# Kernel optimization log

Measured on AMD Instinct MI355X. Metric: run time of the kernel, lower is better.

The kernel has to match this reference:

```python
import jax, jax.numpy as jnp
import numpy as np

PS = 8  # patch_size
EPS = 1e-5


def _layernorm(t, w, b):
    m = jnp.mean(t, axis=-1, keepdims=True)
    v = jnp.mean((t - m) ** 2, axis=-1, keepdims=True)
    return (t - m) * jax.lax.rsqrt(v + EPS) * w + b


def _to3d(t):  # B(HW)C -> BCHW
    B, N, C = t.shape
    H = W = int(np.sqrt(N))
    return t.reshape(B, H, W, C).transpose(0, 3, 1, 2)


def _to2d(t):  # BCHW -> B(HW)C
    B, C, H, W = t.shape
    return t.reshape(B, C, H * W).swapaxes(-1, -2)


def _block(t, ps=PS):  # BCHW -> [B, M, ps*ps, C] (dilated-grid blocking, as in torch code)
    B, C, H, W = t.shape
    t = t.reshape(B, C, ps, H // ps, ps, W // ps)
    t = t.transpose(0, 3, 5, 2, 4, 1)
    return t.reshape(B, (H * W) // (ps * ps), ps * ps, C)


def _unblock(t):  # inverse of _block
    B, M, N, C = t.shape
    Hb = Wb = int(np.sqrt(M))
    ps = int(np.sqrt(N))
    t = t.reshape(B, Hb, Wb, ps, ps, C)
    t = t.transpose(0, 5, 3, 1, 4, 2)
    return t.reshape(B, C, Hb * ps, Wb * ps)


def setup_inputs() -> dict:
    key = jax.random.key(0)
    ks = jax.random.split(key, 8)
    B, N, D, H = 8, 4096, 256, 8
    s = 1.0 / np.sqrt(D)
    return {
        "x": jax.random.normal(ks[0], (B, N, D), jnp.float32),
        "ln1_w": jnp.ones((D,), jnp.float32),
        "ln1_b": jnp.zeros((D,), jnp.float32),
        "q": jax.random.normal(ks[1], (H, D, D), jnp.float32) * s,
        "k": jax.random.normal(ks[2], (D, D), jnp.float32) * s,
        "v": jax.random.normal(ks[3], (D, D), jnp.float32) * s,
        "o": jax.random.normal(ks[4], (H, D, D), jnp.float32) * s,
        "ln2_w": jnp.ones((D,), jnp.float32),
        "ln2_b": jnp.zeros((D,), jnp.float32),
        "w1": jax.random.normal(ks[5], (D, D), jnp.float32) * s,
        "b1": jnp.zeros((D,), jnp.float32),
        "w2": jax.random.normal(ks[6], (D, D), jnp.float32) * s,
        "b2": jnp.zeros((D,), jnp.float32),
    }


def reference(x, ln1_w, ln1_b, q, k, v, o, ln2_w, ln2_b, w1, b1, w2, b2):
    # blocked input: [B, M, P, D], M = HW/ps^2, P = ps^2
    a = _block(_to3d(_layernorm(x, ln1_w, ln1_b)))
    nh = q.shape[0]
    Q = jnp.einsum('bmnd,hdk->bhmnk', a, q)
    Q1, Q2 = Q[:, : nh // 2], Q[:, nh // 2 :]
    K = jnp.einsum('bmnd,dk->bmnk', a, k)
    V = jnp.einsum('bmnd,dv->bmnv', a, v)
    # axis 1: attend across blocks (m) at fixed within-block position (y=n)
    s1 = jax.nn.softmax(jnp.einsum('bhxyk,bzyk->bhyxz', Q1, K), axis=-1)
    O1 = jnp.einsum('bhyxz,bzyv->bhxyv', s1, V)
    # axis 2: attend within block (n) at fixed block (x=m)
    s2 = jax.nn.softmax(jnp.einsum('bhxyk,bxzk->bhxyz', Q2, K), axis=-1)
    O2 = jnp.einsum('bhxyz,bxzv->bhxyv', s2, V)
    O = jnp.concatenate([O1, O2], axis=1)  # [B, H, M, P, D]
    # faithful to torch: 'bhmnd,hdv->bmnd' sums over h and v
    Z = jnp.einsum('bhmnd,hdv->bmnd', O, o)
    x = x + _to2d(_unblock(Z))
    h = _layernorm(x, ln2_w, ln2_b)
    mlp = jax.nn.relu(h @ w1 + b1) @ w2 + b2
    return x + mlp
```

## Files before the change

### kernel.cpp

```cpp
#include <hip/hip_runtime.h>

#define Bc   8
#define Tc   4096
#define Dc   256
#define EPSc 1e-5f

typedef _Float16 half_t;
typedef __attribute__((ext_vector_type(4))) _Float16 half4_t;
typedef __attribute__((ext_vector_type(8))) _Float16 frag8;
typedef __attribute__((ext_vector_type(4))) float f32x4;

#define MFMA_F16(a, b, c) __builtin_amdgcn_mfma_f32_16x16x32_f16((a), (b), (c), 0, 0, 0)

__global__ __launch_bounds__(256) void osum_kernel(const float* __restrict__ o, float* __restrict__ os) {
  int h = blockIdx.x, d = threadIdx.x;
  const float* row = o + ((size_t)h * 256 + d) * 256;
  float s = 0.f;
  #pragma unroll 8
  for (int v = 0; v < 256; v += 4) {
    float4 r4 = *(const float4*)&row[v];
    s += r4.x + r4.y + r4.z + r4.w;
  }
  os[h * 256 + d] = s;
}

__global__ __launch_bounds__(256) void prepM_kernel(const float* __restrict__ q,
                                                    const float* __restrict__ k,
                                                    half_t* __restrict__ Mt) {
  __shared__ float shK[32 * 260];
  __shared__ float shQ[32 * 260];
  int tid = threadIdx.x;
  int h = blockIdx.x >> 6, et = (blockIdx.x >> 3) & 7, dt = blockIdx.x & 7;
  const float* kbase = k + (size_t)(et * 32) * 256;
  const float* qbase = q + ((size_t)h * 256 + dt * 32) * 256;
  #pragma unroll
  for (int r = 0; r < 8; r++) {
    int f = r * 256 + tid;
    int row = f >> 6, c4 = (f & 63) * 4;
    *(float4*)&shK[row * 260 + c4] = *(const float4*)&kbase[(size_t)row * 256 + c4];
    *(float4*)&shQ[row * 260 + c4] = *(const float4*)&qbase[(size_t)row * 256 + c4];
  }
  __syncthreads();
  int e = tid & 31, dg = tid >> 5;
  const float* kr = &shK[e * 260];
  const float* q0 = &shQ[(dg * 4 + 0) * 260];
  const float* q1 = &shQ[(dg * 4 + 1) * 260];
  const float* q2 = &shQ[(dg * 4 + 2) * 260];
  const float* q3 = &shQ[(dg * 4 + 3) * 260];
  float a0 = 0.f, a1 = 0.f, a2 = 0.f, a3 = 0.f;
  #pragma unroll 4
  for (int kk = 0; kk < 256; kk += 4) {
    float4 kv = *(const float4*)&kr[kk];
    float4 v0 = *(const float4*)&q0[kk];
    float4 v1 = *(const float4*)&q1[kk];
    float4 v2 = *(const float4*)&q2[kk];
    float4 v3 = *(const float4*)&q3[kk];
    a0 += v0.x * kv.x + v0.y * kv.y + v0.z * kv.z + v0.w * kv.w;
    a1 += v1.x * kv.x + v1.y * kv.y + v1.z * kv.z + v1.w * kv.w;
    a2 += v2.x * kv.x + v2.y * kv.y + v2.z * kv.z + v2.w * kv.w;
    a3 += v3.x * kv.x + v3.y * kv.y + v3.z * kv.z + v3.w * kv.w;
  }
  half4_t outv;
  outv[0] = (half_t)a0; outv[1] = (half_t)a1; outv[2] = (half_t)a2; outv[3] = (half_t)a3;
  *(half4_t*)&Mt[((size_t)h * 256 + et * 32 + e) * 256 + dt * 32 + dg * 4] = outv;
}

__global__ __launch_bounds__(256) void prepT_kernel(const float* __restrict__ v,
                                                    const float* __restrict__ w1,
                                                    const float* __restrict__ w2,
                                                    half_t* vt, half_t* w1t, half_t* w2t) {
  int which = blockIdx.x >> 8, n = blockIdx.x & 255, d = threadIdx.x;
  const float* src = which == 0 ? v : (which == 1 ? w1 : w2);
  half_t* dst = which == 0 ? vt : (which == 1 ? w1t : w2t);
  dst[(size_t)n * 256 + d] = (half_t)src[(size_t)d * 256 + n];
}

__global__ __launch_bounds__(256) void ln1_kernel(
    const float* __restrict__ x, const float* __restrict__ w,
    const float* __restrict__ bia, half_t* __restrict__ aH) {
  int row  = blockIdx.x * 4 + (threadIdx.x >> 6);
  int lane = threadIdx.x & 63;
  float4 v = *(const float4*)&x[(size_t)row * 256 + lane * 4];
  float s  = v.x + v.y + v.z + v.w;
  float sq = v.x * v.x + v.y * v.y + v.z * v.z + v.w * v.w;
  #pragma unroll
  for (int off = 1; off < 64; off <<= 1) { s += __shfl_xor(s, off); sq += __shfl_xor(sq, off); }
  float mean = s * (1.f / 256), var = sq * (1.f / 256) - mean * mean;
  float r = rsqrtf(var + EPSc);
  float4 wv = *(const float4*)&w[lane * 4];
  float4 bv = *(const float4*)&bia[lane * 4];
  half4_t y;
  y[0] = (half_t)((v.x - mean) * r * wv.x + bv.x);
  y[1] = (half_t)((v.y - mean) * r * wv.y + bv.y);
  y[2] = (half_t)((v.z - mean) * r * wv.z + bv.z);
  y[3] = (half_t)((v.w - mean) * r * wv.w + bv.w);
  int bb = row >> 12, p = row & 4095, hh = p >> 6, ww = p & 63;
  int m = (hh & 7) * 8 + (ww & 7), n = (hh >> 3) * 8 + (ww >> 3);
  *(half4_t*)&aH[((size_t)((bb * 64 + m) * 64 + n)) * 256 + lane * 4] = y;
}

__global__ __launch_bounds__(256, 2) void attn_kernel(
    const half_t* __restrict__ aH, const half_t* __restrict__ Mt,
    const half_t* __restrict__ vt, const float* __restrict__ osum,
    half_t* __restrict__ Z0, half_t* __restrict__ Z1, int gofs) {
  __shared__ half_t shA[64 * 264];
  __shared__ half_t shU[64 * 264 + 64 * 72];
  half_t* shVT = shU;
  half_t* shW  = shU;
  half_t* shP  = shU + 64 * 264;
  int tid = threadIdx.x, lane = tid & 63, w = tid >> 6;
  int l16 = lane & 15, quad = lane >> 4;
  int g = blockIdx.x + gofs;
  int mode = g >> 9, gg = g & 511, b = gg >> 6, slice = gg & 63;
  int hbase = mode * 4;
  half_t* Z = mode ? Z1 : Z0;

  #pragma unroll
  for (int i = 0; i < 8; i++) {
    int slot = i * 256 + tid;
    int z = slot >> 5, c8 = (slot & 31) * 8;
    size_t rz = mode ? ((size_t)(b * 64 + slice) * 64 + z) : ((size_t)(b * 64 + z) * 64 + slice);
    *(frag8*)&shA[z * 264 + c8] = *(const frag8*)&aH[rz * 256 + c8];
  }
  __syncthreads();

  #pragma unroll
  for (int dth = 0; dth < 2; dth++) {
    f32x4 vacc[2][4];
    #pragma unroll
    for (int dt2 = 0; dt2 < 2; dt2++)
      #pragma unroll
      for (int zt = 0; zt < 4; zt++) vacc[dt2][zt] = (f32x4){0.f, 0.f, 0.f, 0.f};
    #pragma unroll
    for (int ks = 0; ks < 8; ks++) {
      int k0 = ks * 32 + quad * 8;
      frag8 vf0 = *(const frag8*)&vt[(size_t)(w * 64 + dth * 32 +  0 + l16) * 256 + k0];
      frag8 vf1 = *(const frag8*)&vt[(size_t)(w * 64 + dth * 32 + 16 + l16) * 256 + k0];
      frag8 bfr[4];
      #pragma unroll
      for (int zt = 0; zt < 4; zt++)
        bfr[zt] = *(const frag8*)&shA[(zt * 16 + l16) * 264 + k0];
      #pragma unroll
      for (int zt = 0; zt < 4; zt++) {
        vacc[0][zt] = MFMA_F16(vf0, bfr[zt], vacc[0][zt]);
        vacc[1][zt] = MFMA_F16(vf1, bfr[zt], vacc[1][zt]);
      }
    }
    #pragma unroll
    for (int dt2 = 0; dt2 < 2; dt2++)
      #pragma unroll
      for (int zt = 0; zt < 4; zt++)
        #pragma unroll
        for (int r = 0; r < 4; r++)
          shVT[(w * 64 + dth * 32 + dt2 * 16 + quad * 4 + r) * 72 + zt * 16 + l16] = (half_t)vacc[dt2][zt][r];
  }
  __syncthreads();

  frag8 vtreg[4][2];
  #pragma unroll
  for (int dt = 0; dt < 4; dt++)
    #pragma unroll
    for (int ks = 0; ks < 2; ks++)
      vtreg[dt][ks] = *(const frag8*)&shVT[(w * 64 + dt * 16 + l16) * 72 + ks * 32 + quad * 8];

  float osv[4][4];
  #pragma unroll
  for (int hh = 0; hh < 4; hh++)
    #pragma unroll
    for (int dt = 0; dt < 4; dt++)
      osv[hh][dt] = osum[(hbase + hh) * 256 + w * 64 + dt * 16 + l16];

  f32x4 zacc[4][4];
  #pragma unroll
  for (int mf = 0; mf < 4; mf++)
    #pragma unroll
    for (int dt = 0; dt < 4; dt++) zacc[mf][dt] = (f32x4){0.f, 0.f, 0.f, 0.f};
  __syncthreads();

  #pragma unroll
  for (int hh = 0; hh < 4; hh++) {
    const half_t* Mth = Mt + (size_t)(hbase + hh) * 65536;
    #pragma unroll
    for (int eh = 0; eh < 2; eh++) {
      f32x4 wacc[2][4];
      #pragma unroll
      for (int et2 = 0; et2 < 2; et2++)
        #pragma unroll
        for (int mf = 0; mf < 4; mf++) wacc[et2][mf] = (f32x4){0.f, 0.f, 0.f, 0.f};
      #pragma unroll
      for (int ks = 0; ks < 8; ks++) {
        int k0 = ks * 32 + quad * 8;
        frag8 bf0 = *(const frag8*)&Mth[(size_t)(w * 64 + eh * 32 +  0 + l16) * 256 + k0];
        frag8 bf1 = *(const frag8*)&Mth[(size_t)(w * 64 + eh * 32 + 16 + l16) * 256 + k0];
        frag8 af[4];
        #pragma unroll
        for (int mf = 0; mf < 4; mf++) af[mf] = *(const frag8*)&shA[(mf * 16 + l16) * 264 + k0];
        #pragma unroll
        for (int mf = 0; mf < 4; mf++) {
          wacc[0][mf] = MFMA_F16(af[mf], bf0, wacc[0][mf]);
          wacc[1][mf] = MFMA_F16(af[mf], bf1, wacc[1][mf]);
        }
      }
      #pragma unroll
      for (int et2 = 0; et2 < 2; et2++)
        #pragma unroll
        for (int mf = 0; mf < 4; mf++)
          #pragma unroll
          for (int r = 0; r < 4; r++)
            shW[(mf * 16 + quad * 4 + r) * 264 + w * 64 + eh * 32 + et2 * 16 + l16] = (half_t)wacc[et2][mf][r];
    }
    __syncthreads();
    {
      f32x4 sacc[4];
      #pragma unroll
      for (int zt = 0; zt < 4; zt++) sacc[zt] = (f32x4){0.f, 0.f, 0.f, 0.f};
      #pragma unroll
      for (int ks = 0; ks < 8; ks++) {
        int k0 = ks * 32 + quad * 8;
        frag8 wf = *(const frag8*)&shW[(w * 16 + l16) * 264 + k0];
        #pragma unroll
        for (int zt = 0; zt < 4; zt++) {
          frag8 kf = *(const frag8*)&shA[(zt * 16 + l16) * 264 + k0];
          sacc[zt] = MFMA_F16(wf, kf, sacc[zt]);
        }
      }
      #pragma unroll
      for (int r = 0; r < 4; r++) {
        float mx = fmaxf(fmaxf(sacc[0][r], sacc[1][r]), fmaxf(sacc[2][r], sacc[3][r]));
        #pragma unroll
        for (int off = 1; off < 16; off <<= 1) mx = fmaxf(mx, __shfl_xor(mx, off));
        float e0 = __expf(sacc[0][r] - mx), e1 = __expf(sacc[1][r] - mx);
        float e2 = __expf(sacc[2][r] - mx), e3 = __expf(sacc[3][r] - mx);
        float sum = e0 + e1 + e2 + e3;
        #pragma unroll
        for (int off = 1; off < 16; off <<= 1) sum += __shfl_xor(sum, off);
        float inv = 1.f / sum;
        int m = w * 16 + quad * 4 + r;
        shP[m * 72 + l16 +  0] = (half_t)(e0 * inv);
        shP[m * 72 + l16 + 16] = (half_t)(e1 * inv);
        shP[m * 72 + l16 + 32] = (half_t)(e2 * inv);
        shP[m * 72 + l16 + 48] = (half_t)(e3 * inv);
      }
    }
    __syncthreads();
    #pragma unroll
    for (int mf = 0; mf < 4; mf++) {
      frag8 pf0 = *(const frag8*)&shP[(mf * 16 + l16) * 72 +  0 + quad * 8];
      frag8 pf1 = *(const frag8*)&shP[(mf * 16 + l16) * 72 + 32 + quad * 8];
      #pragma unroll
      for (int dt = 0; dt < 4; dt++) {
        f32x4 oacc = (f32x4){0.f, 0.f, 0.f, 0.f};
        oacc = MFMA_F16(pf0, vtreg[dt][0], oacc);
        oacc = MFMA_F16(pf1, vtreg[dt][1], oacc);
        #pragma unroll
        for (int r = 0; r < 4; r++) zacc[mf][dt][r] += oacc[r] * osv[hh][dt];
      }
    }
  }

  #pragma unroll
  for (int mf = 0; mf < 4; mf++)
    #pragma unroll
    for (int dt = 0; dt < 4; dt++)
      #pragma unroll
      for (int r = 0; r < 4; r++)
        shA[(mf * 16 + quad * 4 + r) * 264 + w * 64 + dt * 16 + l16] = (half_t)zacc[mf][dt][r];
  __syncthreads();
  #pragma unroll
  for (int i = 0; i < 8; i++) {
    int slot = i * 256 + tid;
    int grow = slot >> 5, c8 = (slot & 31) * 8;
    size_t zrow = mode ? ((size_t)(b * 64 + slice) * 64 + grow) : ((size_t)(b * 64 + grow) * 64 + slice);
    *(frag8*)&Z[zrow * 256 + c8] = *(const frag8*)&shA[grow * 264 + c8];
  }
}

__global__ __launch_bounds__(256, 2) void mlp_kernel(
    const float* __restrict__ x, const half_t* __restrict__ Z0, const half_t* __restrict__ Z1,
    const float* __restrict__ lw, const float* __restrict__ lb,
    const half_t* __restrict__ w1t, const float* __restrict__ b1,
    const half_t* __restrict__ w2t, const float* __restrict__ b2,
    float* __restrict__ out) {
  __shared__ half_t shH[64 * 264];
  __shared__ half_t shHH[64 * 264];
  int tid = threadIdx.x, lane = tid & 63, w = tid >> 6;
  int l16 = lane & 15, quad = lane >> 4;
  int row0 = blockIdx.x * 64;

  #pragma unroll 4
  for (int i = 0; i < 16; i++) {
    int rl = w * 16 + i;
    int row = row0 + rl;
    size_t base = (size_t)row * 256 + lane * 4;
    int bb = row >> 12, p = row & 4095, hh = p >> 6, ww = p & 63;
    int m = (hh & 7) * 8 + (ww & 7), n = (hh >> 3) * 8 + (ww >> 3);
    size_t zbase = ((size_t)((bb * 64 + m) * 64 + n)) * 256 + lane * 4;
    float4 xv = *(const float4*)&x[base];
    half4_t zv0 = *(const half4_t*)&Z0[zbase];
    half4_t zv1 = *(const half4_t*)&Z1[zbase];
    float4 v;
    v.x = xv.x + (float)zv0[0] + (float)zv1[0];
    v.y = xv.y + (float)zv0[1] + (float)zv1[1];
    v.z = xv.z + (float)zv0[2] + (float)zv1[2];
    v.w = xv.w + (float)zv0[3] + (float)zv1[3];
    float s  = v.x + v.y + v.z + v.w;
    float sq = v.x * v.x + v.y * v.y + v.z * v.z + v.w * v.w;
    #pragma unroll
    for (int off = 1; off < 64; off <<= 1) { s += __shfl_xor(s, off); sq += __shfl_xor(sq, off); }
    float mean = s * (1.f / 256), var = sq * (1.f / 256) - mean * mean;
    float r = rsqrtf(var + EPSc);
    float4 wv = *(const float4*)&lw[lane * 4];
    float4 bv = *(const float4*)&lb[lane * 4];
    half4_t y;
    y[0] = (half_t)((v.x - mean) * r * wv.x + bv.x);
    y[1] = (half_t)((v.y - mean) * r * wv.y + bv.y);
    y[2] = (half_t)((v.z - mean) * r * wv.z + bv.z);
    y[3] = (half_t)((v.w - mean) * r * wv.w + bv.w);
    *(half4_t*)&shH[rl * 264 + lane * 4] = y;
  }
  __syncthreads();

  {
    f32x4 acc[4][4];
    #pragma unroll
    for (int mf = 0; mf < 4; mf++)
      #pragma unroll
      for (int nt = 0; nt < 4; nt++) acc[mf][nt] = (f32x4){0.f, 0.f, 0.f, 0.f};
    #pragma unroll
    for (int ks = 0; ks < 8; ks++) {
      int k0 = ks * 32 + quad * 8;
      frag8 af[4], bf[4];
      #pragma unroll
      for (int mf = 0; mf < 4; mf++) af[mf] = *(const frag8*)&shH[(mf * 16 + l16) * 264 + k0];
      #pragma unroll
      for (int nt = 0; nt < 4; nt++)
        bf[nt] = *(const frag8*)&w1t[(size_t)(w * 64 + nt * 16 + l16) * 256 + k0];
      #pragma unroll
      for (int mf = 0; mf < 4; mf++)
        #pragma unroll
        for (int nt = 0; nt < 4; nt++) acc[mf][nt] = MFMA_F16(af[mf], bf[nt], acc[mf][nt]);
    }
    #pragma unroll
    for (int mf = 0; mf < 4; mf++)
      #pragma unroll
      for (int nt = 0; nt < 4; nt++)
        #pragma unroll
        for (int r = 0; r < 4; r++) {
          int rr = mf * 16 + quad * 4 + r, col = w * 64 + nt * 16 + l16;
          float vv = acc[mf][nt][r] + b1[col];
          vv = fmaxf(vv, 0.f);
          shHH[rr * 264 + col] = (half_t)vv;
        }
  }
  __syncthreads();

  {
    f32x4 acc[4][4];
    #pragma unroll
    for (int mf = 0; mf < 4; mf++)
      #pragma unroll
      for (int nt = 0; nt < 4; nt++) acc[mf][nt] = (f32x4){0.f, 0.f, 0.f, 0.f};
    #pragma unroll
    for (int ks = 0; ks < 8; ks++) {
      int k0 = ks * 32 + quad * 8;
      frag8 af[4], bf[4];
      #pragma unroll
      for (int mf = 0; mf < 4; mf++) af[mf] = *(const frag8*)&shHH[(mf * 16 + l16) * 264 + k0];
      #pragma unroll
      for (int nt = 0; nt < 4; nt++)
        bf[nt] = *(const frag8*)&w2t[(size_t)(w * 64 + nt * 16 + l16) * 256 + k0];
      #pragma unroll
      for (int mf = 0; mf < 4; mf++)
        #pragma unroll
        for (int nt = 0; nt < 4; nt++) acc[mf][nt] = MFMA_F16(af[mf], bf[nt], acc[mf][nt]);
    }
    #pragma unroll
    for (int mf = 0; mf < 4; mf++)
      #pragma unroll
      for (int r = 0; r < 4; r++) {
        int rr = mf * 16 + quad * 4 + r;
        int row = row0 + rr;
        int bb = row >> 12, p = row & 4095, hh = p >> 6, ww = p & 63;
        int m = (hh & 7) * 8 + (ww & 7), n = (hh >> 3) * 8 + (ww >> 3);
        size_t zrow = ((size_t)((bb * 64 + m) * 64 + n)) * 256;
        size_t xrow = (size_t)row * 256;
        #pragma unroll
        for (int nt = 0; nt < 4; nt++) {
          int col = w * 64 + nt * 16 + l16;
          float vres = x[xrow + col] + (float)Z0[zrow + col] + (float)Z1[zrow + col];
          float vv = acc[mf][nt][r] + b2[col];
          out[xrow + col] = vv + vres;
        }
      }
  }
}

extern "C" void kernel_launch(void* const* d_in, const int* in_sizes, int n_in,
                              void* d_out, int out_size, void* d_ws, size_t ws_size,
                              hipStream_t stream) {
  (void)in_sizes; (void)n_in; (void)out_size; (void)ws_size;
  const float* x    = (const float*)d_in[0];
  const float* ln1w = (const float*)d_in[1];
  const float* ln1b = (const float*)d_in[2];
  const float* q    = (const float*)d_in[3];
  const float* k    = (const float*)d_in[4];
  const float* v    = (const float*)d_in[5];
  const float* o    = (const float*)d_in[6];
  const float* ln2w = (const float*)d_in[7];
  const float* ln2b = (const float*)d_in[8];
  const float* w1   = (const float*)d_in[9];
  const float* b1   = (const float*)d_in[10];
  const float* w2   = (const float*)d_in[11];
  const float* b2   = (const float*)d_in[12];
  float* out = (float*)d_out;

  const size_t ROWS = (size_t)Bc * Tc;
  const size_t ELTS = ROWS * Dc;
  const size_t MB16 = ELTS * sizeof(half_t);
  char* ws = (char*)d_ws;
  float*  osumB = (float*)ws;
  half_t* Mt    = (half_t*)(ws + (64 << 10));
  half_t* vt    = (half_t*)(ws + (64 << 10) + (1 << 20));
  half_t* w1t   = (half_t*)(ws + (64 << 10) + (1 << 20) + (128 << 10));
  half_t* w2t   = (half_t*)(ws + (64 << 10) + (1 << 20) + (256 << 10));
  half_t* aH    = (half_t*)(ws + (2 << 20));
  half_t* Zb0   = (half_t*)(ws + (2 << 20) + MB16);
  half_t* Zb1   = (half_t*)(ws + (2 << 20) + 2 * MB16);

  osum_kernel <<<8,   256, 0, stream>>>(o, osumB);
  prepM_kernel<<<512, 256, 0, stream>>>(q, k, Mt);
  prepT_kernel<<<768, 256, 0, stream>>>(v, w1, w2, vt, w1t, w2t);
  ln1_kernel  <<<ROWS / 4, 256, 0, stream>>>(x, ln1w, ln1b, aH);
  attn_kernel <<<1024, 256, 0, stream>>>(aH, Mt, vt, osumB, Zb0, Zb1, 0);
  mlp_kernel  <<<ROWS / 64, 256, 0, stream>>>(x, Zb0, Zb1, ln2w, ln2b, w1t, b1, w2t, b2, out);
}
```

Measured before the change: 276.9 us.

## Fuse LayerNorm1 into attention load and merge weight-prep kernels into one launch

```diff
diff --git a/kernel.cpp b/kernel.cpp
--- a/kernel.cpp
+++ b/kernel.cpp
@@ -12,97 +12,71 @@
 
 #define MFMA_F16(a, b, c) __builtin_amdgcn_mfma_f32_16x16x32_f16((a), (b), (c), 0, 0, 0)
 
-__global__ __launch_bounds__(256) void osum_kernel(const float* __restrict__ o, float* __restrict__ os) {
-  int h = blockIdx.x, d = threadIdx.x;
-  const float* row = o + ((size_t)h * 256 + d) * 256;
-  float s = 0.f;
-  #pragma unroll 8
-  for (int v = 0; v < 256; v += 4) {
-    float4 r4 = *(const float4*)&row[v];
-    s += r4.x + r4.y + r4.z + r4.w;
-  }
-  os[h * 256 + d] = s;
-}
-
-__global__ __launch_bounds__(256) void prepM_kernel(const float* __restrict__ q,
-                                                    const float* __restrict__ k,
-                                                    half_t* __restrict__ Mt) {
+__global__ __launch_bounds__(256) void prep_kernel(
+    const float* __restrict__ q, const float* __restrict__ k,
+    const float* __restrict__ v, const float* __restrict__ w1, const float* __restrict__ w2,
+    const float* __restrict__ o,
+    half_t* __restrict__ Mt, half_t* vt, half_t* w1t, half_t* w2t, float* __restrict__ os) {
   __shared__ float shK[32 * 260];
   __shared__ float shQ[32 * 260];
-  int tid = threadIdx.x;
-  int h = blockIdx.x >> 6, et = (blockIdx.x >> 3) & 7, dt = blockIdx.x & 7;
-  const float* kbase = k + (size_t)(et * 32) * 256;
-  const float* qbase = q + ((size_t)h * 256 + dt * 32) * 256;
-  #pragma unroll
-  for (int r = 0; r < 8; r++) {
-    int f = r * 256 + tid;
-    int row = f >> 6, c4 = (f & 63) * 4;
-    *(float4*)&shK[row * 260 + c4] = *(const float4*)&kbase[(size_t)row * 256 + c4];
-    *(float4*)&shQ[row * 260 + c4] = *(const float4*)&qbase[(size_t)row * 256 + c4];
-  }
-  __syncthreads();
-  int e = tid & 31, dg = tid >> 5;
-  const float* kr = &shK[e * 260];
-  const float* q0 = &shQ[(dg * 4 + 0) * 260];
-  const float* q1 = &shQ[(dg * 4 + 1) * 260];
-  const float* q2 = &shQ[(dg * 4 + 2) * 260];
-  const float* q3 = &shQ[(dg * 4 + 3) * 260];
-  float a0 = 0.f, a1 = 0.f, a2 = 0.f, a3 = 0.f;
-  #pragma unroll 4
-  for (int kk = 0; kk < 256; kk += 4) {
-    float4 kv = *(const float4*)&kr[kk];
-    float4 v0 = *(const float4*)&q0[kk];
-    float4 v1 = *(const float4*)&q1[kk];
-    float4 v2 = *(const float4*)&q2[kk];
-    float4 v3 = *(const float4*)&q3[kk];
-    a0 += v0.x * kv.x + v0.y * kv.y + v0.z * kv.z + v0.w * kv.w;
-    a1 += v1.x * kv.x + v1.y * kv.y + v1.z * kv.z + v1.w * kv.w;
-    a2 += v2.x * kv.x + v2.y * kv.y + v2.z * kv.z + v2.w * kv.w;
-    a3 += v3.x * kv.x + v3.y * kv.y + v3.z * kv.z + v3.w * kv.w;
-  }
-  half4_t outv;
-  outv[0] = (half_t)a0; outv[1] = (half_t)a1; outv[2] = (half_t)a2; outv[3] = (half_t)a3;
-  *(half4_t*)&Mt[((size_t)h * 256 + et * 32 + e) * 256 + dt * 32 + dg * 4] = outv;
+  int bid = blockIdx.x, tid = threadIdx.x;
+  if (bid < 512) {
+    int h = bid >> 6, et = (bid >> 3) & 7, dt = bid & 7;
+    const float* kbase = k + (size_t)(et * 32) * 256;
+    const float* qbase = q + ((size_t)h * 256 + dt * 32) * 256;
+    #pragma unroll
+    for (int r = 0; r < 8; r++) {
+      int f = r * 256 + tid;
+      int row = f >> 6, c4 = (f & 63) * 4;
+      *(float4*)&shK[row * 260 + c4] = *(const float4*)&kbase[(size_t)row * 256 + c4];
+      *(float4*)&shQ[row * 260 + c4] = *(const float4*)&qbase[(size_t)row * 256 + c4];
+    }
+    __syncthreads();
+    int e = tid & 31, dg = tid >> 5;
+    const float* kr = &shK[e * 260];
+    const float* q0 = &shQ[(dg * 4 + 0) * 260];
+    const float* q1 = &shQ[(dg * 4 + 1) * 260];
+    const float* q2 = &shQ[(dg * 4 + 2) * 260];
+    const float* q3 = &shQ[(dg * 4 + 3) * 260];
+    float a0 = 0.f, a1 = 0.f, a2 = 0.f, a3 = 0.f;
+    #pragma unroll 4
+    for (int kk = 0; kk < 256; kk += 4) {
+      float4 kv = *(const float4*)&kr[kk];
+      float4 v0 = *(const float4*)&q0[kk];
+      float4 v1 = *(const float4*)&q1[kk];
+      float4 v2 = *(const float4*)&q2[kk];
+      float4 v3 = *(const float4*)&q3[kk];
+      a0 += v0.x * kv.x + v0.y * kv.y + v0.z * kv.z + v0.w * kv.w;
+      a1 += v1.x * kv.x + v1.y * kv.y + v1.z * kv.z + v1.w * kv.w;
+      a2 += v2.x * kv.x + v2.y * kv.y + v2.z * kv.z + v2.w * kv.w;
+      a3 += v3.x * kv.x + v3.y * kv.y + v3.z * kv.z + v3.w * kv.w;
+    }
+    half4_t outv;
+    outv[0] = (half_t)a0; outv[1] = (half_t)a1; outv[2] = (half_t)a2; outv[3] = (half_t)a3;
+    *(half4_t*)&Mt[((size_t)h * 256 + et * 32 + e) * 256 + dt * 32 + dg * 4] = outv;
+  } else if (bid < 1280) {
+    int b2 = bid - 512;
+    int which = b2 >> 8, n = b2 & 255, d = tid;
+    const float* src = which == 0 ? v : (which == 1 ? w1 : w2);
+    half_t* dst = which == 0 ? vt : (which == 1 ? w1t : w2t);
+    dst[(size_t)n * 256 + d] = (half_t)src[(size_t)d * 256 + n];
+  } else {
+    int h = bid - 1280, d = tid;
+    const float* row = o + ((size_t)h * 256 + d) * 256;
+    float s = 0.f;
+    #pragma unroll 8
+    for (int vv = 0; vv < 256; vv += 4) {
+      float4 r4 = *(const float4*)&row[vv];
+      s += r4.x + r4.y + r4.z + r4.w;
+    }
+    os[h * 256 + d] = s;
+  }
 }
 
-__global__ __launch_bounds__(256) void prepT_kernel(const float* __restrict__ v,
-                                                    const float* __restrict__ w1,
-                                                    const float* __restrict__ w2,
-                                                    half_t* vt, half_t* w1t, half_t* w2t) {
-  int which = blockIdx.x >> 8, n = blockIdx.x & 255, d = threadIdx.x;
-  const float* src = which == 0 ? v : (which == 1 ? w1 : w2);
-  half_t* dst = which == 0 ? vt : (which == 1 ? w1t : w2t);
-  dst[(size_t)n * 256 + d] = (half_t)src[(size_t)d * 256 + n];
-}
-
-__global__ __launch_bounds__(256) void ln1_kernel(
-    const float* __restrict__ x, const float* __restrict__ w,
-    const float* __restrict__ bia, half_t* __restrict__ aH) {
-  int row  = blockIdx.x * 4 + (threadIdx.x >> 6);
-  int lane = threadIdx.x & 63;
-  float4 v = *(const float4*)&x[(size_t)row * 256 + lane * 4];
-  float s  = v.x + v.y + v.z + v.w;
-  float sq = v.x * v.x + v.y * v.y + v.z * v.z + v.w * v.w;
-  #pragma unroll
-  for (int off = 1; off < 64; off <<= 1) { s += __shfl_xor(s, off); sq += __shfl_xor(sq, off); }
-  float mean = s * (1.f / 256), var = sq * (1.f / 256) - mean * mean;
-  float r = rsqrtf(var + EPSc);
-  float4 wv = *(const float4*)&w[lane * 4];
-  float4 bv = *(const float4*)&bia[lane * 4];
-  half4_t y;
-  y[0] = (half_t)((v.x - mean) * r * wv.x + bv.x);
-  y[1] = (half_t)((v.y - mean) * r * wv.y + bv.y);
-  y[2] = (half_t)((v.z - mean) * r * wv.z + bv.z);
-  y[3] = (half_t)((v.w - mean) * r * wv.w + bv.w);
-  int bb = row >> 12, p = row & 4095, hh = p >> 6, ww = p & 63;
-  int m = (hh & 7) * 8 + (ww & 7), n = (hh >> 3) * 8 + (ww >> 3);
-  *(half4_t*)&aH[((size_t)((bb * 64 + m) * 64 + n)) * 256 + lane * 4] = y;
-}
-
 __global__ __launch_bounds__(256, 2) void attn_kernel(
-    const half_t* __restrict__ aH, const half_t* __restrict__ Mt,
-    const half_t* __restrict__ vt, const float* __restrict__ osum,
-    half_t* __restrict__ Z0, half_t* __restrict__ Z1, int gofs) {
+    const float* __restrict__ x, const float* __restrict__ lw, const float* __restrict__ lb,
+    const half_t* __restrict__ Mt, const half_t* __restrict__ vt, const float* __restrict__ osum,
+    half_t* __restrict__ Z0, half_t* __restrict__ Z1) {
   __shared__ half_t shA[64 * 264];
   __shared__ half_t shU[64 * 264 + 64 * 72];
   half_t* shVT = shU;
@@ -110,17 +84,40 @@
   half_t* shP  = shU + 64 * 264;
   int tid = threadIdx.x, lane = tid & 63, w = tid >> 6;
   int l16 = lane & 15, quad = lane >> 4;
-  int g = blockIdx.x + gofs;
+  int g = blockIdx.x;
   int mode = g >> 9, gg = g & 511, b = gg >> 6, slice = gg & 63;
   int hbase = mode * 4;
   half_t* Z = mode ? Z1 : Z0;
 
-  #pragma unroll
-  for (int i = 0; i < 8; i++) {
-    int slot = i * 256 + tid;
-    int z = slot >> 5, c8 = (slot & 31) * 8;
-    size_t rz = mode ? ((size_t)(b * 64 + slice) * 64 + z) : ((size_t)(b * 64 + z) * 64 + slice);
-    *(frag8*)&shA[z * 264 + c8] = *(const frag8*)&aH[rz * 256 + c8];
+  {
+    float4 wv4 = *(const float4*)&lw[lane * 4];
+    float4 bv4 = *(const float4*)&lb[lane * 4];
+    float4 xr[16];
+    #pragma unroll
+    for (int i = 0; i < 16; i++) {
+      int z = w * 16 + i;
+      int m = mode ? slice : z, n = mode ? z : slice;
+      int hh = ((n >> 3) << 3) + (m >> 3), ww2 = ((n & 7) << 3) + (m & 7);
+      int trow = b * 4096 + hh * 64 + ww2;
+      xr[i] = *(const float4*)&x[(size_t)trow * 256 + lane * 4];
+    }
+    #pragma unroll
+    for (int i = 0; i < 16; i++) {
+      int z = w * 16 + i;
+      float4 vv = xr[i];
+      float s  = vv.x + vv.y + vv.z + vv.w;
+      float sq = vv.x * vv.x + vv.y * vv.y + vv.z * vv.z + vv.w * vv.w;
+      #pragma unroll
+      for (int off = 1; off < 64; off <<= 1) { s += __shfl_xor(s, off); sq += __shfl_xor(sq, off); }
+      float mean = s * (1.f / 256), var = sq * (1.f / 256) - mean * mean;
+      float r = rsqrtf(var + EPSc);
+      half4_t y;
+      y[0] = (half_t)((vv.x - mean) * r * wv4.x + bv4.x);
+      y[1] = (half_t)((vv.y - mean) * r * wv4.y + bv4.y);
+      y[2] = (half_t)((vv.z - mean) * r * wv4.z + bv4.z);
+      y[3] = (half_t)((vv.w - mean) * r * wv4.w + bv4.w);
+      *(half4_t*)&shA[z * 264 + lane * 4] = y;
+    }
   }
   __syncthreads();
 
@@ -423,14 +420,10 @@
   half_t* vt    = (half_t*)(ws + (64 << 10) + (1 << 20));
   half_t* w1t   = (half_t*)(ws + (64 << 10) + (1 << 20) + (128 << 10));
   half_t* w2t   = (half_t*)(ws + (64 << 10) + (1 << 20) + (256 << 10));
-  half_t* aH    = (half_t*)(ws + (2 << 20));
-  half_t* Zb0   = (half_t*)(ws + (2 << 20) + MB16);
-  half_t* Zb1   = (half_t*)(ws + (2 << 20) + 2 * MB16);
-
-  osum_kernel <<<8,   256, 0, stream>>>(o, osumB);
-  prepM_kernel<<<512, 256, 0, stream>>>(q, k, Mt);
-  prepT_kernel<<<768, 256, 0, stream>>>(v, w1, w2, vt, w1t, w2t);
-  ln1_kernel  <<<ROWS / 4, 256, 0, stream>>>(x, ln1w, ln1b, aH);
-  attn_kernel <<<1024, 256, 0, stream>>>(aH, Mt, vt, osumB, Zb0, Zb1, 0);
+  half_t* Zb0   = (half_t*)(ws + (2 << 20));
+  half_t* Zb1   = (half_t*)(ws + (2 << 20) + MB16);
+
+  prep_kernel <<<1288, 256, 0, stream>>>(q, k, v, w1, w2, o, Mt, vt, w1t, w2t, osumB);
+  attn_kernel <<<1024, 256, 0, stream>>>(x, ln1w, ln1b, Mt, vt, osumB, Zb0, Zb1);
   mlp_kernel  <<<ROWS / 64, 256, 0, stream>>>(x, Zb0, Zb1, ln2w, ln2b, w1t, b1, w2t, b2, out);
 }
```

New measurement: 282.8 us. +2.1%, slower.
